# Kernel tuning notes

Hardware: AMD Instinct MI355X
Metric: run time of the kernel (lower is better)

Reference implementation:

```python
import jax, jax.numpy as jnp
import numpy as np

ALPHA = 0.2
NEG = -9e15
EPS = 1e-5


def _gat(h, adj, W, a, out_features):
    # h: [B,N,Fin], adj: [B,N,N], W: [Fin,Fout], a: [2*Fout,1]
    Wh = jnp.matmul(h, W)                      # [B,N,Fout]
    Wh1 = jnp.matmul(Wh, a[:out_features])     # [B,N,1]
    Wh2 = jnp.matmul(Wh, a[out_features:])     # [B,N,1]
    e = Wh1 + jnp.swapaxes(Wh2, 1, 2)          # [B,N,N]
    e = jax.nn.leaky_relu(e, negative_slope=ALPHA)
    scores = jnp.where(adj > 0, e, NEG)
    att = jax.nn.softmax(scores, axis=1)       # NOTE: dim=1 as in source
    return jnp.matmul(att, Wh)                 # [B,N,Fout]


def _layernorm(x, g, b):
    mu = jnp.mean(x, axis=-1, keepdims=True)
    var = jnp.var(x, axis=-1, keepdims=True)
    return (x - mu) * jax.lax.rsqrt(var + EPS) * g + b


def setup_inputs() -> dict:
    key = jax.random.key(0)
    ks = jax.random.split(key, 8)
    B, N, F, H = 2, 4096, 256, 1024
    x = jax.random.normal(ks[0], (B, N, F), dtype=jnp.float32)
    adj = jax.random.randint(ks[1], (B, N, N), 0, 2, dtype=jnp.int32)
    def xavier(k, shape):
        fan_in, fan_out = shape[0], shape[1]
        lim = np.sqrt(6.0 / (fan_in + fan_out))
        return jax.random.uniform(k, shape, jnp.float32, -lim, lim)
    return {
        "x": x,
        "adj": adj,
        "W1": xavier(ks[2], (F, F)),
        "a1": xavier(ks[3], (2 * F, 1)),
        "W2": xavier(ks[4], (F, F)),
        "a2": xavier(ks[5], (2 * F, 1)),
        "w_ff1": xavier(ks[6], (F, H)) ,
        "b_ff1": jnp.zeros((H,), jnp.float32),
        "w_ff2": xavier(ks[7], (H, F)),
        "b_ff2": jnp.zeros((F,), jnp.float32),
        "g_ln1": jnp.ones((F,), jnp.float32),
        "b_ln1": jnp.zeros((F,), jnp.float32),
        "g_ln2": jnp.ones((F,), jnp.float32),
        "b_ln2": jnp.zeros((F,), jnp.float32),
    }


def reference(x, adj, W1, a1, W2, a2, w_ff1, b_ff1, w_ff2, b_ff2,
              g_ln1, b_ln1, g_ln2, b_ln2):
    Fout = W1.shape[1]
    residual = x
    # dropout is a no-op in eval mode
    h = _gat(x, adj, W1, a1, Fout)          # single head -> cat is identity
    h = _gat(h, adj, W2, a2, W2.shape[1])
    h = _layernorm(residual + h, g_ln1, b_ln1)
    residual2 = h
    ff = jnp.matmul(jax.nn.relu(jnp.matmul(h, w_ff1) + b_ff1), w_ff2) + b_ff2
    return _layernorm(residual2 + ff, g_ln2, b_ln2)
```

## Files before the change

kernel.cpp:

```cpp
#include <hip/hip_runtime.h>
#include <math.h>

#define ALPHA 0.2f
#define NEGV  -9e15f
#define EPSV  1e-5f

constexpr int B_ = 2, N_ = 4096, F_ = 256, H_ = 1024;
constexpr int SPLIT_ = 16;
constexpr int SPLITJ_ = 4;

typedef __attribute__((ext_vector_type(4))) float f32x4;
typedef __attribute__((ext_vector_type(8))) short s16x8;

__device__ __forceinline__ unsigned short f2bf(float f) {
    unsigned u = __builtin_bit_cast(unsigned, f);
    u += 0x7fffu + ((u >> 16) & 1u);
    return (unsigned short)(u >> 16);
}

__global__ __launch_bounds__(256) void zero_kernel(float* __restrict__ p)
{
    const int i = (blockIdx.x * 256 + threadIdx.x) * 4;
    *(float4*)&p[i] = make_float4(0.f, 0.f, 0.f, 0.f);
}

__global__ __launch_bounds__(256) void transp_all_kernel(
    const float* __restrict__ W1, const float* __restrict__ W2,
    const float* __restrict__ F1s, const float* __restrict__ F2s,
    unsigned short* __restrict__ D1, unsigned short* __restrict__ D2,
    unsigned short* __restrict__ D3, unsigned short* __restrict__ D4)
{
    const int mi = blockIdx.z;
    const float* src; unsigned short* dst; int R, Cc;
    if (mi == 0)      { src = W1;  dst = D1; R = 256;  Cc = 256; }
    else if (mi == 1) { src = W2;  dst = D2; R = 256;  Cc = 256; }
    else if (mi == 2) { src = F1s; dst = D3; R = 256;  Cc = 1024; }
    else              { src = F2s; dst = D4; R = 1024; Cc = 256; }
    const int r0 = blockIdx.x * 64, c0 = blockIdx.y * 64;
    if (r0 >= R || c0 >= Cc) return;

    __shared__ float T[64][65];
    const int t = threadIdx.x;
    #pragma unroll
    for (int s = 0; s < 4; ++s) {
        const int rr = s * 16 + (t >> 4);
        const int cq = t & 15;
        const float4 v = *(const float4*)&src[(size_t)(r0 + rr) * Cc + c0 + cq * 4];
        T[rr][cq * 4 + 0] = v.x; T[rr][cq * 4 + 1] = v.y;
        T[rr][cq * 4 + 2] = v.z; T[rr][cq * 4 + 3] = v.w;
    }
    __syncthreads();
    #pragma unroll
    for (int s = 0; s < 4; ++s) {
        const int cr = s * 16 + (t >> 4);
        const int rq = t & 15;
        ushort4 o;
        o.x = f2bf(T[rq * 4 + 0][cr]);
        o.y = f2bf(T[rq * 4 + 1][cr]);
        o.z = f2bf(T[rq * 4 + 2][cr]);
        o.w = f2bf(T[rq * 4 + 3][cr]);
        *(ushort4*)&dst[(size_t)(c0 + cr) * R + r0 + rq * 4] = o;
    }
}

__global__ __launch_bounds__(256) void gemm128_kernel(
    const void* __restrict__ Ap, const unsigned short* __restrict__ Wt,
    const float* __restrict__ bias, void* __restrict__ Cp,
    unsigned short* __restrict__ Tout, const float* __restrict__ wha,
    float* __restrict__ Wh1, float* __restrict__ Wh2,
    int Nc, int K, int relu, int a_bf16, int c_mode)
{
    __shared__ unsigned short As[128 * 72];
    __shared__ unsigned short Bs[128 * 72];
    const int t = threadIdx.x;
    const int w = t >> 6, l = t & 63;
    const int quad = l >> 4, l15 = l & 15;
    const int wr = w & 1, wc = w >> 1;
    const int row0 = blockIdx.y * 128, col0 = blockIdx.x * 128;
    const int sr = t >> 1;
    const int sk = (t & 1) * 32;

    f32x4 acc[4][4];
    #pragma unroll
    for (int it = 0; it < 4; ++it)
        #pragma unroll
        for (int ft = 0; ft < 4; ++ft) acc[it][ft] = (f32x4)(0.f);

    for (int k0 = 0; k0 < K; k0 += 64) {
        if (a_bf16) {
            const unsigned short* ap =
                (const unsigned short*)Ap + (size_t)(row0 + sr) * K + k0 + sk;
            #pragma unroll
            for (int u = 0; u < 4; ++u)
                *(s16x8*)&As[sr * 72 + sk + u * 8] = *(const s16x8*)(ap + u * 8);
        } else {
            const float* ap = (const float*)Ap + (size_t)(row0 + sr) * K + k0 + sk;
            #pragma unroll
            for (int u = 0; u < 8; ++u) {
                const float4 v = *(const float4*)(ap + u * 4);
                ushort4 o;
                o.x = f2bf(v.x); o.y = f2bf(v.y); o.z = f2bf(v.z); o.w = f2bf(v.w);
                *(ushort4*)&As[sr * 72 + sk + u * 4] = o;
            }
        }
        {
            const unsigned short* bp = Wt + (size_t)(col0 + sr) * K + k0 + sk;
            #pragma unroll
            for (int u = 0; u < 4; ++u)
                *(s16x8*)&Bs[sr * 72 + sk + u * 8] = *(const s16x8*)(bp + u * 8);
        }
        __syncthreads();
        #pragma unroll
        for (int ks = 0; ks < 64; ks += 32) {
            s16x8 af[4], bf[4];
            #pragma unroll
            for (int it = 0; it < 4; ++it)
                af[it] = *(const s16x8*)&As[(wr * 64 + it * 16 + l15) * 72 + ks + quad * 8];
            #pragma unroll
            for (int ft = 0; ft < 4; ++ft)
                bf[ft] = *(const s16x8*)&Bs[(wc * 64 + ft * 16 + l15) * 72 + ks + quad * 8];
            #pragma unroll
            for (int ft = 0; ft < 4; ++ft)
                #pragma unroll
                for (int it = 0; it < 4; ++it)
                    acc[it][ft] = __builtin_amdgcn_mfma_f32_16x16x32_bf16(
                        af[it], bf[ft], acc[it][ft], 0, 0, 0);
        }
        __syncthreads();
    }

    if (c_mode) {
        #pragma unroll
        for (int ft = 0; ft < 4; ++ft) {
            const int col = col0 + wc * 64 + ft * 16 + l15;
            const float bv = bias ? bias[col] : 0.f;
            #pragma unroll
            for (int it = 0; it < 4; ++it) {
                const int rbase = row0 + wr * 64 + it * 16 + quad * 4;
                #pragma unroll
                for (int rr = 0; rr < 4; ++rr) {
                    float v = acc[it][ft][rr] + bv;
                    if (relu) v = fmaxf(v, 0.f);
                    if (c_mode == 2)
                        ((unsigned short*)Cp)[(size_t)(rbase + rr) * Nc + col] = f2bf(v);
                    else
                        ((float*)Cp)[(size_t)(rbase + rr) * Nc + col] = v;
                }
            }
        }
    }

    if (Tout) {
        const int bb = row0 >> 12;
        #pragma unroll
        for (int ft = 0; ft < 4; ++ft) {
            const int col = col0 + wc * 64 + ft * 16 + l15;
            #pragma unroll
            for (int it = 0; it < 4; ++it) {
                const int ibase = (row0 & (N_ - 1)) + wr * 64 + it * 16 + quad * 4;
                ushort4 o;
                o.x = f2bf(acc[it][ft][0]); o.y = f2bf(acc[it][ft][1]);
                o.z = f2bf(acc[it][ft][2]); o.w = f2bf(acc[it][ft][3]);
                *(ushort4*)&Tout[((size_t)bb * F_ + col) * N_ + ibase] = o;
            }
        }
    }

    if (wha) {
        float a1v[4], a2v[4];
        #pragma unroll
        for (int ft = 0; ft < 4; ++ft) {
            const int col = col0 + wc * 64 + ft * 16 + l15;
            a1v[ft] = wha[col];
            a2v[ft] = wha[F_ + col];
        }
        #pragma unroll
        for (int it = 0; it < 4; ++it)
            #pragma unroll
            for (int rr = 0; rr < 4; ++rr) {
                float s1 = 0.f, s2 = 0.f;
                #pragma unroll
                for (int ft = 0; ft < 4; ++ft) {
                    s1 += acc[it][ft][rr] * a1v[ft];
                    s2 += acc[it][ft][rr] * a2v[ft];
                }
                #pragma unroll
                for (int mkk = 1; mkk < 16; mkk <<= 1) {
                    s1 += __shfl_xor(s1, mkk);
                    s2 += __shfl_xor(s2, mkk);
                }
                if (l15 == 0) {
                    const int row = row0 + wr * 64 + it * 16 + quad * 4 + rr;
                    atomicAdd(&Wh1[row], s1);
                    atomicAdd(&Wh2[row], s2);
                }
            }
    }
}

__global__ __launch_bounds__(256) void colstats_adj_kernel(
    const int* __restrict__ adj, unsigned long long* __restrict__ maskOut,
    const float* __restrict__ Wh1, const float* __restrict__ Wh2,
    float* __restrict__ pM, float* __restrict__ pS)
{
    const int t = threadIdx.x;
    const int j = blockIdx.x * 256 + t;
    const int sp = blockIdx.y;
    const int b = blockIdx.z;
    const int i0 = sp * (N_ / SPLIT_);
    const int w = t >> 6, l = t & 63;
    const float w2 = Wh2[b * N_ + j];
    const float* __restrict__ w1p = Wh1 + b * N_ + i0;
    const int* __restrict__ ap = adj + ((size_t)b * N_ + i0) * N_ + j;

    float m = -3.4e38f, s = 0.f;
    for (int c = 0; c < N_ / SPLIT_; c += 8) {
        int v[8];
        #pragma unroll
        for (int u = 0; u < 8; ++u) v[u] = ap[(size_t)(c + u) * N_];
        float x[8];
        #pragma unroll
        for (int u = 0; u < 8; ++u) {
            const bool act = v[u] > 0;
            const unsigned long long bm = __ballot(act);
            if (l == 0)
                maskOut[((size_t)b * N_ + i0 + c + u) * (N_ / 64) + blockIdx.x * 4 + w] = bm;
            const float e0 = w1p[c + u] + w2;
            const float e = fmaxf(e0, ALPHA * e0);
            x[u] = act ? e : NEGV;
        }
        const float cm = fmaxf(fmaxf(fmaxf(x[0], x[1]), fmaxf(x[2], x[3])),
                               fmaxf(fmaxf(x[4], x[5]), fmaxf(x[6], x[7])));
        const float nm = fmaxf(m, cm);
        float cs = 0.f;
        #pragma unroll
        for (int u = 0; u < 8; ++u) cs += __expf(x[u] - nm);
        s = s * __expf(m - nm) + cs;
        m = nm;
    }
    pM[((size_t)b * SPLIT_ + sp) * N_ + j] = m;
    pS[((size_t)b * SPLIT_ + sp) * N_ + j] = s;
}

__global__ __launch_bounds__(256) void colstats3_kernel(
    const unsigned long long* __restrict__ mask,
    const float* __restrict__ Wh1, const float* __restrict__ Wh2,
    float* __restrict__ pM, float* __restrict__ pS)
{
    const int t = threadIdx.x;
    const int j = blockIdx.x * 256 + t;
    const int sp = blockIdx.y;
    const int b = blockIdx.z;
    const int i0 = sp * (N_ / SPLIT_);
    const int w = t >> 6;
    const int jbit = t & 63;
    const float w2 = Wh2[b * N_ + j];
    const unsigned long long* __restrict__ mbase =
        mask + ((size_t)b * N_ + i0) * (N_ / 64) + blockIdx.x * 4 + w;
    const float* __restrict__ w1p = Wh1 + b * N_ + i0;

    float m = -3.4e38f, s = 0.f;
    for (int c = 0; c < N_ / SPLIT_; c += 8) {
        float x[8];
        #pragma unroll
        for (int u = 0; u < 8; ++u) {
            const unsigned long long mw = mbase[(size_t)(c + u) * (N_ / 64)];
            const float e0 = w1p[c + u] + w2;
            const float e = fmaxf(e0, ALPHA * e0);
            x[u] = ((mw >> jbit) & 1ull) ? e : NEGV;
        }
        const float cm = fmaxf(fmaxf(fmaxf(x[0], x[1]), fmaxf(x[2], x[3])),
                               fmaxf(fmaxf(x[4], x[5]), fmaxf(x[6], x[7])));
        const float nm = fmaxf(m, cm);
        float cs = 0.f;
        #pragma unroll
        for (int u = 0; u < 8; ++u) cs += __expf(x[u] - nm);
        s = s * __expf(m - nm) + cs;
        m = nm;
    }
    pM[((size_t)b * SPLIT_ + sp) * N_ + j] = m;
    pS[((size_t)b * SPLIT_ + sp) * N_ + j] = s;
}

__global__ __launch_bounds__(256) void colfin2_kernel(
    const float* __restrict__ pM, const float* __restrict__ pS,
    float* __restrict__ Mo)
{
    const int j = blockIdx.x * 256 + threadIdx.x;
    const int b = blockIdx.y;
    float m = -3.4e38f;
    #pragma unroll
    for (int s = 0; s < SPLIT_; ++s)
        m = fmaxf(m, pM[((size_t)b * SPLIT_ + s) * N_ + j]);
    float sum = 0.f;
    #pragma unroll
    for (int s = 0; s < SPLIT_; ++s)
        sum += pS[((size_t)b * SPLIT_ + s) * N_ + j] *
               __expf(pM[((size_t)b * SPLIT_ + s) * N_ + j] - m);
    Mo[b * N_ + j] = m + logf(sum);
}

__global__ __launch_bounds__(256) void att_mfma3_kernel(
    const unsigned short* __restrict__ mask16, const unsigned short* __restrict__ Wht,
    const float* __restrict__ Wh1, const float* __restrict__ Wh2,
    const float* __restrict__ Mo, float* __restrict__ part)
{
    __shared__ unsigned short Bs[256 * 72];
    __shared__ unsigned short Ps[64 * 72];
    __shared__ float w2s[1024];
    __shared__ float mos[1024];

    const int t = threadIdx.x;
    const int w = t >> 6, l = t & 63;
    const int quad = l >> 4, l15 = l & 15;
    const int b = blockIdx.z;
    const int i0 = blockIdx.x * 64;
    const int sp = blockIdx.y;
    const int jbase = sp * (N_ / SPLITJ_);

    const int pi = t >> 2;
    const int pj4 = t & 3;
    const float w1i = Wh1[b * N_ + i0 + pi];
    const unsigned short* __restrict__ mrow =
        mask16 + ((size_t)b * N_ + i0 + pi) * (N_ / 16);
    const unsigned short* __restrict__ WhtB = Wht + (size_t)b * F_ * N_;

    {
        const float4 a = *(const float4*)&Wh2[b * N_ + jbase + t * 4];
        const float4 c = *(const float4*)&Mo[b * N_ + jbase + t * 4];
        *(float4*)&w2s[t * 4] = a;
        *(float4*)&mos[t * 4] = c;
    }

    f32x4 acc[4][4];
    #pragma unroll
    for (int it = 0; it < 4; ++it)
        #pragma unroll
        for (int ft = 0; ft < 4; ++ft) acc[it][ft] = (f32x4)(0.f);

    const int f0s = t >> 3;
    const int prt = (t & 7) * 8;
    s16x8 breg[8];
    {
        const int jb = jbase;
        #pragma unroll
        for (int s = 0; s < 8; ++s)
            breg[s] = *(const s16x8*)&WhtB[(size_t)(f0s + s * 32) * N_ + jb + prt];
    }
    unsigned short mb_cur = mrow[jbase / 16 + pj4];
    __syncthreads();

    constexpr int NITER = (N_ / SPLITJ_) / 64;
    for (int itr = 0; itr < NITER; ++itr) {
        const int jb = jbase + itr * 64;
        #pragma unroll
        for (int s = 0; s < 8; ++s)
            *(s16x8*)&Bs[(f0s + s * 32) * 72 + prt] = breg[s];
        {
            const unsigned mb = mb_cur;
            const int jl = itr * 64 + pj4 * 16;
            #pragma unroll
            for (int u4 = 0; u4 < 4; ++u4) {
                const float4 w2v = *(const float4*)&w2s[jl + u4 * 4];
                const float4 mov = *(const float4*)&mos[jl + u4 * 4];
                ushort4 o;
                unsigned short* op = &o.x;
                #pragma unroll
                for (int u = 0; u < 4; ++u) {
                    const float xw = w1i + (&w2v.x)[u];
                    const float e = fmaxf(xw, ALPHA * xw);
                    const float x2 = ((mb >> (u4 * 4 + u)) & 1u) ? e : NEGV;
                    op[u] = f2bf(__expf(x2 - (&mov.x)[u]));
                }
                *(ushort4*)&Ps[pi * 72 + pj4 * 16 + u4 * 4] = o;
            }
        }
        __syncthreads();
        if (itr + 1 < NITER) {
            const int jn = jb + 64;
            #pragma unroll
            for (int s = 0; s < 8; ++s)
                breg[s] = *(const s16x8*)&WhtB[(size_t)(f0s + s * 32) * N_ + jn + prt];
            mb_cur = mrow[jn / 16 + pj4];
        }
        #pragma unroll
        for (int ks = 0; ks < 64; ks += 32) {
            s16x8 af[4];
            #pragma unroll
            for (int it = 0; it < 4; ++it)
                af[it] = *(const s16x8*)&Ps[(it * 16 + l15) * 72 + ks + quad * 8];
            #pragma unroll
            for (int ft = 0; ft < 4; ++ft) {
                const s16x8 bf =
                    *(const s16x8*)&Bs[(w * 64 + ft * 16 + l15) * 72 + ks + quad * 8];
                #pragma unroll
                for (int it = 0; it < 4; ++it)
                    acc[it][ft] = __builtin_amdgcn_mfma_f32_16x16x32_bf16(
                        af[it], bf, acc[it][ft], 0, 0, 0);
            }
        }
        __syncthreads();
    }

    float* __restrict__ pout = part + ((size_t)sp * B_ + b) * N_ * F_;
    #pragma unroll
    for (int it = 0; it < 4; ++it)
        #pragma unroll
        for (int ft = 0; ft < 4; ++ft) {
            const int col = w * 64 + ft * 16 + l15;
            #pragma unroll
            for (int rr = 0; rr < 4; ++rr) {
                const int row = i0 + it * 16 + quad * 4 + rr;
                pout[(size_t)row * F_ + col] = acc[it][ft][rr];
            }
        }
}

__global__ __launch_bounds__(256) void reduce4b_kernel(
    const float* __restrict__ p, unsigned short* __restrict__ outb)
{
    const size_t i = ((size_t)blockIdx.x * 256 + threadIdx.x) * 4;
    const size_t S = (size_t)B_ * N_ * F_;
    const float4 a = *(const float4*)&p[i];
    const float4 b = *(const float4*)&p[i + S];
    const float4 c = *(const float4*)&p[i + 2 * S];
    const float4 d = *(const float4*)&p[i + 3 * S];
    ushort4 o;
    o.x = f2bf(a.x + b.x + c.x + d.x);
    o.y = f2bf(a.y + b.y + c.y + d.y);
    o.z = f2bf(a.z + b.z + c.z + d.z);
    o.w = f2bf(a.w + b.w + c.w + d.w);
    *(ushort4*)&outb[i] = o;
}

__global__ __launch_bounds__(256) void addln4_kernel(
    const float* __restrict__ X, const float* __restrict__ p,
    const float* __restrict__ g, const float* __restrict__ bta,
    float* __restrict__ outf, unsigned short* __restrict__ outb)
{
    const int row = blockIdx.x;
    const int t = threadIdx.x;
    const size_t idx = (size_t)row * F_ + t;
    const size_t S = (size_t)B_ * N_ * F_;
    const float v = X[idx] + p[idx] + p[idx + S] + p[idx + 2 * S] + p[idx + 3 * S];
    float s1 = v, s2 = v * v;
    #pragma unroll
    for (int off = 32; off > 0; off >>= 1) {
        s1 += __shfl_down(s1, off);
        s2 += __shfl_down(s2, off);
    }
    __shared__ float r1[4], r2[4];
    __shared__ float mu_s, rs_s;
    const int wid = t >> 6, lane = t & 63;
    if (lane == 0) { r1[wid] = s1; r2[wid] = s2; }
    __syncthreads();
    if (t == 0) {
        const float a = r1[0] + r1[1] + r1[2] + r1[3];
        const float q = r2[0] + r2[1] + r2[2] + r2[3];
        const float mu = a * (1.f / F_);
        const float var = q * (1.f / F_) - mu * mu;
        mu_s = mu;
        rs_s = rsqrtf(var + EPSV);
    }
    __syncthreads();
    const float r = (v - mu_s) * rs_s * g[t] + bta[t];
    outf[idx] = r;
    outb[idx] = f2bf(r);
}

__global__ __launch_bounds__(256) void addln_kernel(
    const float* __restrict__ X, const float* __restrict__ Y,
    const float* __restrict__ g, const float* __restrict__ bta,
    float* __restrict__ out)
{
    const int row = blockIdx.x;
    const int t = threadIdx.x;
    const size_t idx = (size_t)row * F_ + t;
    const float v = X[idx] + Y[idx];
    float s1 = v, s2 = v * v;
    #pragma unroll
    for (int off = 32; off > 0; off >>= 1) {
        s1 += __shfl_down(s1, off);
        s2 += __shfl_down(s2, off);
    }
    __shared__ float r1[4], r2[4];
    __shared__ float mu_s, rs_s;
    const int wid = t >> 6, lane = t & 63;
    if (lane == 0) { r1[wid] = s1; r2[wid] = s2; }
    __syncthreads();
    if (t == 0) {
        const float a = r1[0] + r1[1] + r1[2] + r1[3];
        const float q = r2[0] + r2[1] + r2[2] + r2[3];
        const float mu = a * (1.f / F_);
        const float var = q * (1.f / F_) - mu * mu;
        mu_s = mu;
        rs_s = rsqrtf(var + EPSV);
    }
    __syncthreads();
    out[idx] = (v - mu_s) * rs_s * g[t] + bta[t];
}

extern "C" void kernel_launch(void* const* d_in, const int* in_sizes, int n_in,
                              void* d_out, int out_size, void* d_ws, size_t ws_size,
                              hipStream_t stream)
{
    const float* x     = (const float*)d_in[0];
    const int*   adj   = (const int*)d_in[1];
    const float* W1    = (const float*)d_in[2];
    const float* a1    = (const float*)d_in[3];
    const float* W2    = (const float*)d_in[4];
    const float* a2    = (const float*)d_in[5];
    const float* w_ff1 = (const float*)d_in[6];
    const float* b_ff1 = (const float*)d_in[7];
    const float* w_ff2 = (const float*)d_in[8];
    const float* b_ff2 = (const float*)d_in[9];
    const float* g_ln1 = (const float*)d_in[10];
    const float* b_ln1 = (const float*)d_in[11];
    const float* g_ln2 = (const float*)d_in[12];
    const float* b_ln2 = (const float*)d_in[13];
    float* out = (float*)d_out;

    const int Rtot = B_ * N_;
    char* wsb = (char*)d_ws;
    float* part  = (float*)wsb;
    float* ln1   = (float*)(wsb + 33554432);
    float* ffout = (float*)(wsb + 41943040);
    unsigned short* mid  = (unsigned short*)(wsb + 50331648);
    unsigned short* ln1b = (unsigned short*)(wsb + 67108864);
    unsigned short* g1b  = (unsigned short*)(wsb + 71303168);
    unsigned short* Wht  = (unsigned short*)(wsb + 75497472);
    unsigned long long* mask = (unsigned long long*)(wsb + 79691776);
    unsigned short* mask16 = (unsigned short*)mask;
    unsigned short* Wt1  = (unsigned short*)(wsb + 83886080);
    unsigned short* Wt2  = Wt1 + 65536;
    unsigned short* Wtf1 = Wt2 + 65536;
    unsigned short* Wtf2 = Wtf1 + 262144;
    float* WhA1 = (float*)(wsb + 85196800);
    float* WhA2 = WhA1 + 8192;
    float* WhB1 = WhA2 + 8192;
    float* WhB2 = WhB1 + 8192;
    float* Mo   = (float*)(wsb + 85327872);
    float* pM   = (float*)(wsb + 85360640);
    float* pS   = (float*)(wsb + 85884928);

    const dim3 statsG(N_ / 256, SPLIT_, B_);
    const dim3 finG(N_ / 256, B_);
    const dim3 attG(N_ / 64, SPLITJ_, B_);

    zero_kernel<<<32, 256, 0, stream>>>(WhA1);
    transp_all_kernel<<<dim3(16, 16, 4), 256, 0, stream>>>(
        W1, W2, w_ff1, w_ff2, Wt1, Wt2, Wtf1, Wtf2);

    gemm128_kernel<<<dim3(2, 64), 256, 0, stream>>>(
        x, Wt1, nullptr, nullptr, Wht, a1, WhA1, WhA2, F_, F_, 0, 0, 0);
    colstats_adj_kernel<<<statsG, 256, 0, stream>>>(adj, mask, WhA1, WhA2, pM, pS);
    colfin2_kernel<<<finG, 256, 0, stream>>>(pM, pS, Mo);
    att_mfma3_kernel<<<attG, 256, 0, stream>>>(mask16, Wht, WhA1, WhA2, Mo, part);
    reduce4b_kernel<<<2048, 256, 0, stream>>>(part, g1b);

    gemm128_kernel<<<dim3(2, 64), 256, 0, stream>>>(
        g1b, Wt2, nullptr, nullptr, Wht, a2, WhB1, WhB2, F_, F_, 0, 1, 0);
    colstats3_kernel<<<statsG, 256, 0, stream>>>(mask, WhB1, WhB2, pM, pS);
    colfin2_kernel<<<finG, 256, 0, stream>>>(pM, pS, Mo);
    att_mfma3_kernel<<<attG, 256, 0, stream>>>(mask16, Wht, WhB1, WhB2, Mo, part);

    addln4_kernel<<<Rtot, 256, 0, stream>>>(x, part, g_ln1, b_ln1, ln1, ln1b);

    gemm128_kernel<<<dim3(8, 64), 256, 0, stream>>>(
        ln1b, Wtf1, b_ff1, mid, nullptr, nullptr, nullptr, nullptr, H_, F_, 1, 1, 2);
    gemm128_kernel<<<dim3(2, 64), 256, 0, stream>>>(
        mid, Wtf2, b_ff2, ffout, nullptr, nullptr, nullptr, nullptr, F_, H_, 0, 1, 1);

    addln_kernel<<<Rtot, 256, 0, stream>>>(ln1, ffout, g_ln2, b_ln2, out);
}
```

Measured before the change: 423.6 us.

## Fuse softmax finalize into attention, load Wh directly, store bf16 partials

Folds the zero kernel into the transpose launch and the column-softmax finalize into the attention kernel, which now recomputes the log-sum-exp from the split partials per block. The attention kernel drops its LDS staging of Wh and reads MFMA B fragments straight from global memory. It also writes split-j partial results as bf16 instead of fp32, halving partial-buffer traffic for the reduce and add-layernorm kernels. The trade-offs are redundant finalize work in every block, uncoalesced global B loads with no prefetch, and extra rounding of the partial sums.

```diff
diff --git a/kernel.cpp b/kernel.cpp
--- a/kernel.cpp
+++ b/kernel.cpp
@@ -17,20 +17,28 @@
     u += 0x7fffu + ((u >> 16) & 1u);
     return (unsigned short)(u >> 16);
 }
-
-__global__ __launch_bounds__(256) void zero_kernel(float* __restrict__ p)
-{
-    const int i = (blockIdx.x * 256 + threadIdx.x) * 4;
-    *(float4*)&p[i] = make_float4(0.f, 0.f, 0.f, 0.f);
+__device__ __forceinline__ float bf2f(unsigned short h) {
+    unsigned u = ((unsigned)h) << 16;
+    return __builtin_bit_cast(float, u);
 }
 
 __global__ __launch_bounds__(256) void transp_all_kernel(
     const float* __restrict__ W1, const float* __restrict__ W2,
     const float* __restrict__ F1s, const float* __restrict__ F2s,
     unsigned short* __restrict__ D1, unsigned short* __restrict__ D2,
-    unsigned short* __restrict__ D3, unsigned short* __restrict__ D4)
+    unsigned short* __restrict__ D3, unsigned short* __restrict__ D4,
+    float* __restrict__ zeroDst)
 {
     const int mi = blockIdx.z;
+    const int t = threadIdx.x;
+    if (mi == 4) {
+        const int bid = blockIdx.y * 16 + blockIdx.x;
+        if (bid < 32) {
+            const int i = (bid * 256 + t) * 4;
+            *(float4*)&zeroDst[i] = make_float4(0.f, 0.f, 0.f, 0.f);
+        }
+        return;
+    }
     const float* src; unsigned short* dst; int R, Cc;
     if (mi == 0)      { src = W1;  dst = D1; R = 256;  Cc = 256; }
     else if (mi == 1) { src = W2;  dst = D2; R = 256;  Cc = 256; }
@@ -40,7 +48,6 @@
     if (r0 >= R || c0 >= Cc) return;
 
     __shared__ float T[64][65];
-    const int t = threadIdx.x;
     #pragma unroll
     for (int s = 0; s < 4; ++s) {
         const int rr = s * 16 + (t >> 4);
@@ -282,30 +289,12 @@
     pS[((size_t)b * SPLIT_ + sp) * N_ + j] = s;
 }
 
-__global__ __launch_bounds__(256) void colfin2_kernel(
-    const float* __restrict__ pM, const float* __restrict__ pS,
-    float* __restrict__ Mo)
-{
-    const int j = blockIdx.x * 256 + threadIdx.x;
-    const int b = blockIdx.y;
-    float m = -3.4e38f;
-    #pragma unroll
-    for (int s = 0; s < SPLIT_; ++s)
-        m = fmaxf(m, pM[((size_t)b * SPLIT_ + s) * N_ + j]);
-    float sum = 0.f;
-    #pragma unroll
-    for (int s = 0; s < SPLIT_; ++s)
-        sum += pS[((size_t)b * SPLIT_ + s) * N_ + j] *
-               __expf(pM[((size_t)b * SPLIT_ + s) * N_ + j] - m);
-    Mo[b * N_ + j] = m + logf(sum);
-}
-
-__global__ __launch_bounds__(256) void att_mfma3_kernel(
+__global__ __launch_bounds__(256, 4) void att_dir_kernel(
     const unsigned short* __restrict__ mask16, const unsigned short* __restrict__ Wht,
     const float* __restrict__ Wh1, const float* __restrict__ Wh2,
-    const float* __restrict__ Mo, float* __restrict__ part)
-{
-    __shared__ unsigned short Bs[256 * 72];
+    const float* __restrict__ pM, const float* __restrict__ pS,
+    unsigned short* __restrict__ partb)
+{
     __shared__ unsigned short Ps[64 * 72];
     __shared__ float w2s[1024];
     __shared__ float mos[1024];
@@ -326,10 +315,31 @@
     const unsigned short* __restrict__ WhtB = Wht + (size_t)b * F_ * N_;
 
     {
-        const float4 a = *(const float4*)&Wh2[b * N_ + jbase + t * 4];
-        const float4 c = *(const float4*)&Mo[b * N_ + jbase + t * 4];
-        *(float4*)&w2s[t * 4] = a;
-        *(float4*)&mos[t * 4] = c;
+        const int jg = jbase + t * 4;
+        float4 m4 = make_float4(-3.4e38f, -3.4e38f, -3.4e38f, -3.4e38f);
+        #pragma unroll
+        for (int s = 0; s < SPLIT_; ++s) {
+            const float4 v = *(const float4*)&pM[((size_t)b * SPLIT_ + s) * N_ + jg];
+            m4.x = fmaxf(m4.x, v.x); m4.y = fmaxf(m4.y, v.y);
+            m4.z = fmaxf(m4.z, v.z); m4.w = fmaxf(m4.w, v.w);
+        }
+        float4 s4 = make_float4(0.f, 0.f, 0.f, 0.f);
+        #pragma unroll
+        for (int s = 0; s < SPLIT_; ++s) {
+            const float4 vm = *(const float4*)&pM[((size_t)b * SPLIT_ + s) * N_ + jg];
+            const float4 vs = *(const float4*)&pS[((size_t)b * SPLIT_ + s) * N_ + jg];
+            s4.x += vs.x * __expf(vm.x - m4.x);
+            s4.y += vs.y * __expf(vm.y - m4.y);
+            s4.z += vs.z * __expf(vm.z - m4.z);
+            s4.w += vs.w * __expf(vm.w - m4.w);
+        }
+        float4 mo4;
+        mo4.x = m4.x + __logf(s4.x);
+        mo4.y = m4.y + __logf(s4.y);
+        mo4.z = m4.z + __logf(s4.z);
+        mo4.w = m4.w + __logf(s4.w);
+        *(float4*)&mos[t * 4] = mo4;
+        *(float4*)&w2s[t * 4] = *(const float4*)&Wh2[b * N_ + jg];
     }
 
     f32x4 acc[4][4];
@@ -338,24 +348,13 @@
         #pragma unroll
         for (int ft = 0; ft < 4; ++ft) acc[it][ft] = (f32x4)(0.f);
 
-    const int f0s = t >> 3;
-    const int prt = (t & 7) * 8;
-    s16x8 breg[8];
-    {
-        const int jb = jbase;
-        #pragma unroll
-        for (int s = 0; s < 8; ++s)
-            breg[s] = *(const s16x8*)&WhtB[(size_t)(f0s + s * 32) * N_ + jb + prt];
-    }
     unsigned short mb_cur = mrow[jbase / 16 + pj4];
+    unsigned short mb_next = 0;
     __syncthreads();
 
     constexpr int NITER = (N_ / SPLITJ_) / 64;
     for (int itr = 0; itr < NITER; ++itr) {
         const int jb = jbase + itr * 64;
-        #pragma unroll
-        for (int s = 0; s < 8; ++s)
-            *(s16x8*)&Bs[(f0s + s * 32) * 72 + prt] = breg[s];
         {
             const unsigned mb = mb_cur;
             const int jl = itr * 64 + pj4 * 16;
@@ -376,33 +375,30 @@
             }
         }
         __syncthreads();
-        if (itr + 1 < NITER) {
-            const int jn = jb + 64;
-            #pragma unroll
-            for (int s = 0; s < 8; ++s)
-                breg[s] = *(const s16x8*)&WhtB[(size_t)(f0s + s * 32) * N_ + jn + prt];
-            mb_cur = mrow[jn / 16 + pj4];
-        }
+        if (itr + 1 < NITER) mb_next = mrow[(jb + 64) / 16 + pj4];
         #pragma unroll
         for (int ks = 0; ks < 64; ks += 32) {
+            s16x8 bf[4];
+            #pragma unroll
+            for (int ft = 0; ft < 4; ++ft)
+                bf[ft] = *(const s16x8*)&WhtB[(size_t)(w * 64 + ft * 16 + l15) * N_
+                                              + jb + ks + quad * 8];
             s16x8 af[4];
             #pragma unroll
             for (int it = 0; it < 4; ++it)
                 af[it] = *(const s16x8*)&Ps[(it * 16 + l15) * 72 + ks + quad * 8];
             #pragma unroll
-            for (int ft = 0; ft < 4; ++ft) {
-                const s16x8 bf =
-                    *(const s16x8*)&Bs[(w * 64 + ft * 16 + l15) * 72 + ks + quad * 8];
+            for (int ft = 0; ft < 4; ++ft)
                 #pragma unroll
                 for (int it = 0; it < 4; ++it)
                     acc[it][ft] = __builtin_amdgcn_mfma_f32_16x16x32_bf16(
-                        af[it], bf, acc[it][ft], 0, 0, 0);
-            }
+                        af[it], bf[ft], acc[it][ft], 0, 0, 0);
         }
         __syncthreads();
-    }
-
-    float* __restrict__ pout = part + ((size_t)sp * B_ + b) * N_ * F_;
+        mb_cur = mb_next;
+    }
+
+    unsigned short* __restrict__ pout = partb + ((size_t)sp * B_ + b) * N_ * F_;
     #pragma unroll
     for (int it = 0; it < 4; ++it)
         #pragma unroll
@@ -411,30 +407,35 @@
             #pragma unroll
             for (int rr = 0; rr < 4; ++rr) {
                 const int row = i0 + it * 16 + quad * 4 + rr;
-                pout[(size_t)row * F_ + col] = acc[it][ft][rr];
+                pout[(size_t)row * F_ + col] = f2bf(acc[it][ft][rr]);
             }
         }
 }
 
-__global__ __launch_bounds__(256) void reduce4b_kernel(
-    const float* __restrict__ p, unsigned short* __restrict__ outb)
-{
-    const size_t i = ((size_t)blockIdx.x * 256 + threadIdx.x) * 4;
+__global__ __launch_bounds__(256) void reduceb_kernel(
+    const unsigned short* __restrict__ p, unsigned short* __restrict__ outb)
+{
+    const size_t i = ((size_t)blockIdx.x * 256 + threadIdx.x) * 8;
     const size_t S = (size_t)B_ * N_ * F_;
-    const float4 a = *(const float4*)&p[i];
-    const float4 b = *(const float4*)&p[i + S];
-    const float4 c = *(const float4*)&p[i + 2 * S];
-    const float4 d = *(const float4*)&p[i + 3 * S];
-    ushort4 o;
-    o.x = f2bf(a.x + b.x + c.x + d.x);
-    o.y = f2bf(a.y + b.y + c.y + d.y);
-    o.z = f2bf(a.z + b.z + c.z + d.z);
-    o.w = f2bf(a.w + b.w + c.w + d.w);
-    *(ushort4*)&outb[i] = o;
+    float acc[8] = {};
+    #pragma unroll
+    for (int u = 0; u < 4; ++u) {
+        const ushort4 a = *(const ushort4*)&p[i + u * S];
+        const ushort4 c = *(const ushort4*)&p[i + u * S + 4];
+        acc[0] += bf2f(a.x); acc[1] += bf2f(a.y);
+        acc[2] += bf2f(a.z); acc[3] += bf2f(a.w);
+        acc[4] += bf2f(c.x); acc[5] += bf2f(c.y);
+        acc[6] += bf2f(c.z); acc[7] += bf2f(c.w);
+    }
+    ushort4 o0, o1;
+    o0.x = f2bf(acc[0]); o0.y = f2bf(acc[1]); o0.z = f2bf(acc[2]); o0.w = f2bf(acc[3]);
+    o1.x = f2bf(acc[4]); o1.y = f2bf(acc[5]); o1.z = f2bf(acc[6]); o1.w = f2bf(acc[7]);
+    *(ushort4*)&outb[i] = o0;
+    *(ushort4*)&outb[i + 4] = o1;
 }
 
 __global__ __launch_bounds__(256) void addln4_kernel(
-    const float* __restrict__ X, const float* __restrict__ p,
+    const float* __restrict__ X, const unsigned short* __restrict__ pb,
     const float* __restrict__ g, const float* __restrict__ bta,
     float* __restrict__ outf, unsigned short* __restrict__ outb)
 {
@@ -442,7 +443,8 @@
     const int t = threadIdx.x;
     const size_t idx = (size_t)row * F_ + t;
     const size_t S = (size_t)B_ * N_ * F_;
-    const float v = X[idx] + p[idx] + p[idx + S] + p[idx + 2 * S] + p[idx + 3 * S];
+    const float v = X[idx] + bf2f(pb[idx]) + bf2f(pb[idx + S])
+                  + bf2f(pb[idx + 2 * S]) + bf2f(pb[idx + 3 * S]);
     float s1 = v, s2 = v * v;
     #pragma unroll
     for (int off = 32; off > 0; off >>= 1) {
@@ -522,49 +524,44 @@
 
     const int Rtot = B_ * N_;
     char* wsb = (char*)d_ws;
-    float* part  = (float*)wsb;
-    float* ln1   = (float*)(wsb + 33554432);
-    float* ffout = (float*)(wsb + 41943040);
-    unsigned short* mid  = (unsigned short*)(wsb + 50331648);
-    unsigned short* ln1b = (unsigned short*)(wsb + 67108864);
-    unsigned short* g1b  = (unsigned short*)(wsb + 71303168);
-    unsigned short* Wht  = (unsigned short*)(wsb + 75497472);
-    unsigned long long* mask = (unsigned long long*)(wsb + 79691776);
+    unsigned short* partb = (unsigned short*)wsb;
+    float* ln1   = (float*)(wsb + 16777216);
+    float* ffout = (float*)(wsb + 25165824);
+    unsigned short* mid  = (unsigned short*)(wsb + 33554432);
+    unsigned short* ln1b = (unsigned short*)(wsb + 50331648);
+    unsigned short* g1b  = (unsigned short*)(wsb + 54525952);
+    unsigned short* Wht  = (unsigned short*)(wsb + 58720256);
+    unsigned long long* mask = (unsigned long long*)(wsb + 62914560);
     unsigned short* mask16 = (unsigned short*)mask;
-    unsigned short* Wt1  = (unsigned short*)(wsb + 83886080);
+    unsigned short* Wt1  = (unsigned short*)(wsb + 67108864);
     unsigned short* Wt2  = Wt1 + 65536;
     unsigned short* Wtf1 = Wt2 + 65536;
     unsigned short* Wtf2 = Wtf1 + 262144;
-    float* WhA1 = (float*)(wsb + 85196800);
+    float* WhA1 = (float*)(wsb + 69206016);
     float* WhA2 = WhA1 + 8192;
     float* WhB1 = WhA2 + 8192;
     float* WhB2 = WhB1 + 8192;
-    float* Mo   = (float*)(wsb + 85327872);
-    float* pM   = (float*)(wsb + 85360640);
-    float* pS   = (float*)(wsb + 85884928);
+    float* pM   = (float*)(wsb + 69337088);
+    float* pS   = (float*)(wsb + 69861376);
 
     const dim3 statsG(N_ / 256, SPLIT_, B_);
-    const dim3 finG(N_ / 256, B_);
     const dim3 attG(N_ / 64, SPLITJ_, B_);
 
-    zero_kernel<<<32, 256, 0, stream>>>(WhA1);
-    transp_all_kernel<<<dim3(16, 16, 4), 256, 0, stream>>>(
-        W1, W2, w_ff1, w_ff2, Wt1, Wt2, Wtf1, Wtf2);
+    transp_all_kernel<<<dim3(16, 16, 5), 256, 0, stream>>>(
+        W1, W2, w_ff1, w_ff2, Wt1, Wt2, Wtf1, Wtf2, WhA1);
 
     gemm128_kernel<<<dim3(2, 64), 256, 0, stream>>>(
         x, Wt1, nullptr, nullptr, Wht, a1, WhA1, WhA2, F_, F_, 0, 0, 0);
     colstats_adj_kernel<<<statsG, 256, 0, stream>>>(adj, mask, WhA1, WhA2, pM, pS);
-    colfin2_kernel<<<finG, 256, 0, stream>>>(pM, pS, Mo);
-    att_mfma3_kernel<<<attG, 256, 0, stream>>>(mask16, Wht, WhA1, WhA2, Mo, part);
-    reduce4b_kernel<<<2048, 256, 0, stream>>>(part, g1b);
+    att_dir_kernel<<<attG, 256, 0, stream>>>(mask16, Wht, WhA1, WhA2, pM, pS, partb);
+    reduceb_kernel<<<1024, 256, 0, stream>>>(partb, g1b);
 
     gemm128_kernel<<<dim3(2, 64), 256, 0, stream>>>(
         g1b, Wt2, nullptr, nullptr, Wht, a2, WhB1, WhB2, F_, F_, 0, 1, 0);
     colstats3_kernel<<<statsG, 256, 0, stream>>>(mask, WhB1, WhB2, pM, pS);
-    colfin2_kernel<<<finG, 256, 0, stream>>>(pM, pS, Mo);
-    att_mfma3_kernel<<<attG, 256, 0, stream>>>(mask16, Wht, WhB1, WhB2, Mo, part);
-
-    addln4_kernel<<<Rtot, 256, 0, stream>>>(x, part, g_ln1, b_ln1, ln1, ln1b);
+    att_dir_kernel<<<attG, 256, 0, stream>>>(mask16, Wht, WhB1, WhB2, pM, pS, partb);
+
+    addln4_kernel<<<Rtot, 256, 0, stream>>>(x, partb, g_ln1, b_ln1, ln1, ln1b);
 
     gemm128_kernel<<<dim3(8, 64), 256, 0, stream>>>(
         ln1b, Wtf1, b_ff1, mid, nullptr, nullptr, nullptr, nullptr, H_, F_, 1, 1, 2);
```

Result: slower. 460.4 us (+8.7%).
